# Performance work log

Measured on AMD Instinct MI355X. Metric: run time of the kernel, lower is better.

## Reference

```python
import jax, jax.numpy as jnp
import numpy as np

N, C, H, W, D = 2, 64, 256, 256, 2   # batch, dim, height, width, depth
NW, HEADS, TOPK, KVW = 8, 8, 4, 4    # n_win, num_heads, topk, kv_per_win


def _conv(x, w, b, pad, groups=1):
    # x: NCHW, w: OIHW
    y = jax.lax.conv_general_dilated(
        x, w, (1, 1), [(pad, pad), (pad, pad)],
        dimension_numbers=('NCHW', 'OIHW', 'NCHW'), feature_group_count=groups)
    return y if b is None else y + b[None, :, None, None]


def _ln(x, g, b):
    m = x.mean(-1, keepdims=True)
    v = ((x - m) ** 2).mean(-1, keepdims=True)
    return (x - m) * jax.lax.rsqrt(v + 1e-6) * g + b


def setup_inputs() -> dict:
    key = jax.random.key(0)
    ks = iter(jax.random.split(key, 32))
    def rn(shape, s=0.05):
        return jax.random.normal(next(ks), shape, jnp.float32) * s
    inp = {'x': jax.random.normal(next(ks), (N, C, H, W), jnp.float32)}
    inp.update(
        pos_w=rn((D, C, 1, 3, 3)), pos_b=jnp.zeros((D, C), jnp.float32),
        ln1_g=jnp.ones((D, C), jnp.float32), ln1_b=jnp.zeros((D, C), jnp.float32),
        qkv_w=rn((D, C, 3 * C)), qkv_b=jnp.zeros((D, 3 * C), jnp.float32),
        lepe_w=rn((D, C, 1, 5, 5)), lepe_b=jnp.zeros((D, C), jnp.float32),
        wo_w=rn((D, C, C)), wo_b=jnp.zeros((D, C), jnp.float32),
        ln2_g=jnp.ones((D, C), jnp.float32), ln2_b=jnp.zeros((D, C), jnp.float32),
        fc1_w=rn((D, C, 4 * C)), fc1_b=jnp.zeros((D, 4 * C), jnp.float32),
        pw_w=rn((D, 2 * C, 2 * C, 1, 1)),
        dw_w=rn((D, 2 * C, 1, 3, 3)), dw_b=jnp.zeros((D, 2 * C), jnp.float32),
        fc2_w=rn((D, 2 * C, C)), fc2_b=jnp.zeros((D, C), jnp.float32))
    return inp


def _attn(y, qkv_w, qkv_b, lepe_w, lepe_b, wo_w, wo_b):
    # Bi-level routing attention. y: NHWC
    n, h, w, c = y.shape
    hw, ww = h // NW, w // NW          # window size (32x32)
    p2 = NW * NW                        # number of windows (64)
    hd = c // HEADS
    scale = c ** -0.5                   # qk_dim ** -0.5
    qkv = y @ qkv_w + qkv_b             # (n,h,w,3c)
    q, kimg, vimg = jnp.split(qkv, 3, -1)

    def win(t):  # (n,h,w,c) -> (n,p2,hw,ww,c)
        return t.reshape(n, NW, hw, NW, ww, c).transpose(0, 1, 3, 2, 4, 5).reshape(n, p2, hw, ww, c)

    qw, kw, vw = win(q), win(kimg), win(vimg)
    # region-level routing: window-mean q/k, top-k windows per query window
    q_win = qw.mean((2, 3))
    k_win = kw.mean((2, 3))
    logits = jnp.einsum('npc,nqc->npq', q_win * scale, k_win)
    _, r_idx = jax.lax.top_k(logits, TOPK)           # (n,p2,topk) hard routing (mul_weight='none')
    # kv downsample: adaptive avg pool each 32x32 window to 4x4
    kv = jnp.concatenate([kw, vw], -1)               # (n,p2,hw,ww,2c)
    kvp = kv.reshape(n, p2, KVW, hw // KVW, KVW, ww // KVW, 2 * c).mean((3, 5))
    kvp = kvp.reshape(n, p2, KVW * KVW, 2 * c)       # (n,p2,16,2c)
    # gather top-k windows' kv tokens
    kv_sel = jax.vmap(lambda t, i: t[i])(kvp, r_idx)  # (n,p2,topk,16,2c)
    k_sel, v_sel = jnp.split(kv_sel, 2, -1)
    kt = TOPK * KVW * KVW                             # 64 kv tokens per window
    k_sel = k_sel.reshape(n, p2, kt, HEADS, hd)
    v_sel = v_sel.reshape(n, p2, kt, HEADS, hd)
    qp = qw.reshape(n, p2, hw * ww, HEADS, hd)
    att = jax.nn.softmax(jnp.einsum('npqhc,npkhc->nphqk', qp * scale, k_sel), -1)
    out = jnp.einsum('nphqk,npkhc->npqhc', att, v_sel).reshape(n, p2, hw, ww, c)
    out = out.reshape(n, NW, NW, hw, ww, c).transpose(0, 1, 3, 2, 4, 5).reshape(n, h, w, c)
    # LePE: depthwise 5x5 conv on v over the full image
    lepe = _conv(vimg.transpose(0, 3, 1, 2), lepe_w, lepe_b, 2, groups=c).transpose(0, 2, 3, 1)
    return (out + lepe) @ wo_w + wo_b


def _glu(y, fc1_w, fc1_b, pw_w, dw_w, dw_b, fc2_w, fc2_b):
    # BConvolutionalGLU. y: NHWC
    t = y @ fc1_w + fc1_b                 # (n,h,w,4c)
    xh, vh = jnp.split(t, 2, -1)          # each 2c
    xh = xh.transpose(0, 3, 1, 2)         # NCHW
    xh = _conv(xh, pw_w, None, 0)                           # BSConvU pointwise (no bias)
    xh = _conv(xh, dw_w, dw_b, 1, groups=dw_w.shape[0])     # BSConvU depthwise 3x3
    xh = jax.nn.gelu(xh, approximate=False) * vh.transpose(0, 3, 1, 2)
    return xh.transpose(0, 2, 3, 1) @ fc2_w + fc2_b


def reference(x, pos_w, pos_b, ln1_g, ln1_b, qkv_w, qkv_b, lepe_w, lepe_b,
              wo_w, wo_b, ln2_g, ln2_b, fc1_w, fc1_b, pw_w, dw_w, dw_b,
              fc2_w, fc2_b):
    for i in range(D):
        x = x + _conv(x, pos_w[i], pos_b[i], 1, groups=x.shape[1])
        y = x.transpose(0, 2, 3, 1)  # NHWC
        y = y + _attn(_ln(y, ln1_g[i], ln1_b[i]), qkv_w[i], qkv_b[i],
                      lepe_w[i], lepe_b[i], wo_w[i], wo_b[i])
        y = y + _glu(_ln(y, ln2_g[i], ln2_b[i]), fc1_w[i], fc1_b[i],
                     pw_w[i], dw_w[i], dw_b[i], fc2_w[i], fc2_b[i])
        x = y.transpose(0, 3, 1, 2)  # NCHW
    return x
```

## Files before the change

### kernel.cpp

```cpp
#include <hip/hip_runtime.h>
#include <hip/hip_bf16.h>

typedef __hip_bfloat16 bf16;
typedef __attribute__((ext_vector_type(8))) short short8v;
typedef __attribute__((ext_vector_type(4))) float f32x4;

static constexpr int Nn = 2, Hh = 256, Wd = 256;
static constexpr int Pp = Nn * Hh * Wd;

__device__ inline void sto(float* p, size_t i, float v) { p[i] = v; }
__device__ inline void sto(bf16* p, size_t i, float v) { p[i] = __float2bfloat16(v); }
__device__ inline void ld4(const float* p, float f[4]) {
  const float4 v = *(const float4*)p;
  f[0] = v.x; f[1] = v.y; f[2] = v.z; f[3] = v.w;
}
__device__ inline void ld4(const bf16* p, float f[4]) {
  uint2 u = *(const uint2*)p;
  f[0] = __uint_as_float(u.x << 16); f[1] = __uint_as_float(u.x & 0xffff0000u);
  f[2] = __uint_as_float(u.y << 16); f[3] = __uint_as_float(u.y & 0xffff0000u);
}
__device__ inline void st4(float* p, const float f[4]) {
  *(float4*)p = make_float4(f[0], f[1], f[2], f[3]);
}
__device__ inline void st4(bf16* p, const float f[4]) {
  union { bf16 h[4]; uint2 u; } x;
  x.h[0] = __float2bfloat16(f[0]); x.h[1] = __float2bfloat16(f[1]);
  x.h[2] = __float2bfloat16(f[2]); x.h[3] = __float2bfloat16(f[3]);
  *(uint2*)p = x.u;
}
__device__ inline uint2 pk4(float a, float b, float c, float d) {
  union { bf16 h[4]; uint2 u; } x;
  x.h[0] = __float2bfloat16(a); x.h[1] = __float2bfloat16(b);
  x.h[2] = __float2bfloat16(c); x.h[3] = __float2bfloat16(d);
  return x.u;
}

__global__ void __launch_bounds__(256) k_in_tr(const float* __restrict__ xin,
                                               float* __restrict__ X) {
  __shared__ float t[64][65];
  int blk = blockIdx.x;
  int wt = blk & 3, h = (blk >> 2) & 255, n = blk >> 10;
  int w0 = wt * 64;
  int tx = threadIdx.x & 63, ty = threadIdx.x >> 6;
  const float* src = xin + ((size_t)n * 64 * 256 + h) * 256 + w0;
#pragma unroll
  for (int cc = 0; cc < 16; cc++) {
    int c = cc * 4 + ty;
    t[c][tx] = src[(size_t)c * 65536 + tx];
  }
  __syncthreads();
  float* dst = X + (size_t)(n * 65536 + h * 256 + w0) * 64;
#pragma unroll
  for (int jj = 0; jj < 16; jj++) {
    int j = jj * 4 + ty;
    dst[(size_t)j * 64 + tx] = t[tx][j];
  }
}

__global__ void __launch_bounds__(256) k_out(const float* __restrict__ X,
                                             float* __restrict__ out) {
  __shared__ float t[64][65];
  int blk = blockIdx.x;
  int wt = blk & 3, h = (blk >> 2) & 255, n = blk >> 10;
  int w0 = wt * 64;
  int tx = threadIdx.x & 63, ty = threadIdx.x >> 6;
  const float* src = X + (size_t)(n * 65536 + h * 256 + w0) * 64;
#pragma unroll
  for (int jj = 0; jj < 16; jj++) {
    int j = jj * 4 + ty;
    t[tx][j] = src[(size_t)j * 64 + tx];
  }
  __syncthreads();
  float* dst = out + ((size_t)n * 64 * 256 + h) * 256 + w0;
#pragma unroll
  for (int cc = 0; cc < 16; cc++) {
    int c = cc * 4 + ty;
    dst[(size_t)c * 65536 + tx] = t[c][tx];
  }
}

__global__ void __launch_bounds__(256) k_pcln4(const float* __restrict__ X,
                                               float* __restrict__ A, float* __restrict__ T,
                                               bf16* __restrict__ Tb,
                                               const float* __restrict__ pw,
                                               const float* __restrict__ pb,
                                               const float* __restrict__ g,
                                               const float* __restrict__ b) {
  __shared__ float w9[9][68];
  __shared__ float bb[64];
  int tid = threadIdx.x;
  for (int j = tid; j < 576; j += 256) {
    int tap = j >> 6, c = j & 63;
    w9[tap][c] = pw[c * 9 + tap];
  }
  if (tid < 64) bb[tid] = pb[tid];
  __syncthreads();
  int gid = blockIdx.x * 256 + tid;
  int cg = gid & 15, pg = gid >> 4;
  int c0 = cg << 2;
  int w0 = (pg & 63) << 2, h = (pg >> 6) & 255, n = pg >> 14;
  int pbase = (n << 16) | (h << 8) | w0;
  float acc[4][4];
  {
    const float4 b4 = *(const float4*)&bb[c0];
#pragma unroll
    for (int px = 0; px < 4; px++) {
      acc[px][0] = b4.x; acc[px][1] = b4.y; acc[px][2] = b4.z; acc[px][3] = b4.w;
    }
  }
  float xc[4][4];
#pragma unroll
  for (int ky = 0; ky < 3; ky++) {
    int hh = h + ky - 1;
    if ((unsigned)hh >= 256u) continue;
    const float* xrow = X + (size_t)((n << 16) | (hh << 8)) * 64 + c0;
    float v[6][4];
#pragma unroll
    for (int dx = 0; dx < 6; dx++) {
      int ww = w0 + dx - 1;
      if ((unsigned)ww < 256u) ld4(xrow + (size_t)ww * 64, v[dx]);
      else { v[dx][0] = 0.f; v[dx][1] = 0.f; v[dx][2] = 0.f; v[dx][3] = 0.f; }
    }
    if (ky == 1) {
#pragma unroll
      for (int px = 0; px < 4; px++)
#pragma unroll
        for (int j = 0; j < 4; j++) xc[px][j] = v[px + 1][j];
    }
#pragma unroll
    for (int kx = 0; kx < 3; kx++) {
      const float4 wv = *(const float4*)&w9[ky * 3 + kx][c0];
#pragma unroll
      for (int px = 0; px < 4; px++) {
        acc[px][0] += wv.x * v[px + kx][0]; acc[px][1] += wv.y * v[px + kx][1];
        acc[px][2] += wv.z * v[px + kx][2]; acc[px][3] += wv.w * v[px + kx][3];
      }
    }
  }
  const float4 g4 = *(const float4*)&g[c0];
  const float4 b4 = *(const float4*)&b[c0];
#pragma unroll
  for (int px = 0; px < 4; px++) {
    float a[4];
#pragma unroll
    for (int j = 0; j < 4; j++) a[j] = xc[px][j] + acc[px][j];
    st4(A + (size_t)(pbase + px) * 64 + c0, a);
    float s = a[0] + a[1] + a[2] + a[3];
#pragma unroll
    for (int off = 8; off; off >>= 1) s += __shfl_xor(s, off);
    float mean = s * (1.f / 64.f);
    float d[4], q = 0.f;
#pragma unroll
    for (int j = 0; j < 4; j++) { d[j] = a[j] - mean; q += d[j] * d[j]; }
#pragma unroll
    for (int off = 8; off; off >>= 1) q += __shfl_xor(q, off);
    float inv = rsqrtf(q * (1.f / 64.f) + 1e-6f);
    float y[4] = {d[0] * inv * g4.x + b4.x, d[1] * inv * g4.y + b4.y,
                  d[2] * inv * g4.z + b4.z, d[3] * inv * g4.w + b4.w};
    st4(T + (size_t)(pbase + px) * 64 + c0, y);
    st4(Tb + (size_t)(pbase + px) * 64 + c0, y);
  }
}

__global__ void __launch_bounds__(256) k_lnb4(const float* __restrict__ In,
                                              bf16* __restrict__ Out,
                                              const float* __restrict__ g,
                                              const float* __restrict__ b) {
  int gid = blockIdx.x * 256 + threadIdx.x;
  int pix = gid >> 4, cq = (gid & 15) << 2;
  float a[4];
  ld4(In + (size_t)pix * 64 + cq, a);
  float s = a[0] + a[1] + a[2] + a[3];
#pragma unroll
  for (int off = 8; off; off >>= 1) s += __shfl_xor(s, off);
  float mean = s * (1.f / 64.f);
  float d[4], q = 0.f;
#pragma unroll
  for (int j = 0; j < 4; j++) { d[j] = a[j] - mean; q += d[j] * d[j]; }
#pragma unroll
  for (int off = 8; off; off >>= 1) q += __shfl_xor(q, off);
  float inv = rsqrtf(q * (1.f / 64.f) + 1e-6f);
  const float4 g4 = *(const float4*)&g[cq];
  const float4 b4 = *(const float4*)&b[cq];
  float y[4] = {d[0] * inv * g4.x + b4.x, d[1] * inv * g4.y + b4.y,
                d[2] * inv * g4.z + b4.z, d[3] * inv * g4.w + b4.w};
  st4(Out + (size_t)pix * 64 + cq, y);
}

__global__ void k_prep1(const float* __restrict__ qkvw, const float* __restrict__ qkvb,
                        const float* __restrict__ wow, const float* __restrict__ f2w,
                        bf16* __restrict__ WTq, bf16* __restrict__ WTo,
                        bf16* __restrict__ WT2, float* __restrict__ qbs) {
  int t = blockIdx.x * 256 + threadIdx.x;
  if (t < 8192) {
    int r = t >> 6, k = t & 63;
    int src = r < 64 ? r : r + 64;
    float v = qkvw[k * 192 + src];
    if (r < 64) v *= 0.125f;
    WTq[t] = __float2bfloat16(v);
  } else if (t < 12288) {
    int t2 = t - 8192;
    int r = t2 >> 6, k = t2 & 63;
    WTo[t2] = __float2bfloat16(wow[k * 64 + r]);
  } else if (t < 20480) {
    int t2 = t - 12288;
    int r = t2 >> 7, k = t2 & 127;
    WT2[t2] = __float2bfloat16(f2w[k * 64 + r]);
  }
  if (t < 64) qbs[t] = qkvb[t] * 0.125f;
}

__global__ void k_combine(const float* __restrict__ f1w, const float* __restrict__ f1b,
                          const float* __restrict__ pww, float* __restrict__ Wc,
                          float* __restrict__ bc) {
  int t = blockIdx.x * blockDim.x + threadIdx.x;
  if (t >= 8192) return;
  int o = t & 127, k = t >> 7;
  float acc = 0.f;
  for (int j = 0; j < 128; j++) acc += f1w[k * 256 + j] * pww[o * 128 + j];
  Wc[k * 128 + o] = acc;
  if (k == 0) {
    float b = 0.f;
    for (int j = 0; j < 128; j++) b += f1b[j] * pww[o * 128 + j];
    bc[o] = b;
  }
}

__global__ void k_prep2(const float* __restrict__ f1w, const float* __restrict__ Wc,
                        bf16* __restrict__ WTf1) {
  int t = blockIdx.x * 256 + threadIdx.x;
  if (t >= 16384) return;
  int r = t >> 6, k = t & 63;
  float v = r < 128 ? f1w[k * 256 + 128 + r] : Wc[k * 128 + (r - 128)];
  WTf1[t] = __float2bfloat16(v);
}

template <int K, int N1, int N2, typename TO1, typename TO2, bool RES>
__global__ void __launch_bounds__(256) k_mf(const bf16* __restrict__ In,
                                            const bf16* __restrict__ WT,
                                            const float* __restrict__ b1,
                                            const float* __restrict__ b2,
                                            const float* __restrict__ Res,
                                            TO1* __restrict__ O1, TO2* __restrict__ O2) {
  constexpr int NC = N1 + N2;
  constexpr int KS = K / 32;
  constexpr int NTW = NC / 64;
  constexpr int KB = K * 2;
  constexpr int CH = NC * K / 8;
  __shared__ char lw[NC * K * 2];
  int tid = threadIdx.x;
  for (int ch = tid; ch < CH; ch += 256) {
    int r = ch / (K / 8), cg = ch % (K / 8);
    int byte = (r * KB + cg * 16) ^ ((r & 7) << 4);
    *(uint4*)(lw + byte) = *(const uint4*)((const short*)WT + ch * 8);
  }
  __syncthreads();
  int wid = tid >> 6, lane = tid & 63;
  int lr = lane & 15, lg = lane >> 4;
  int mb = blockIdx.x * 128;
#pragma unroll 2
  for (int ms = 0; ms < 8; ms++) {
    int m0 = mb + ms * 16;
    short8v a[KS];
#pragma unroll
    for (int ks = 0; ks < KS; ks++)
      a[ks] = *(const short8v*)((const short*)In + (size_t)(m0 + lr) * K + ks * 32 + lg * 8);
#pragma unroll
    for (int t = 0; t < NTW; t++) {
      int nt = wid * NTW + t;
      int col = nt * 16 + lr;
      float bv = (N2 == 0 || col < N1) ? b1[col] : b2[col - N1];
      f32x4 acc = {bv, bv, bv, bv};
#pragma unroll
      for (int ks = 0; ks < KS; ks++) {
        int byte = (col * KB + ks * 64 + lg * 16) ^ ((col & 7) << 4);
        short8v bfrag = *(const short8v*)(lw + byte);
        acc = __builtin_amdgcn_mfma_f32_16x16x32_bf16(a[ks], bfrag, acc, 0, 0, 0);
      }
      int r0 = m0 + lg * 4;
#pragma unroll
      for (int j = 0; j < 4; j++) {
        float v = acc[j];
        size_t row = r0 + j;
        if (RES) v += Res[row * N1 + col];
        if (N2 == 0 || col < N1) sto(O1, row * N1 + col, v);
        else sto(O2, row * N2 + (col - N1), v);
      }
    }
  }
}

__global__ void k_pool8(const float* __restrict__ T, float* __restrict__ Y8) {
  int b = blockIdx.x;
  int c = threadIdx.x;
  int bx = b & 31, by = (b >> 5) & 31, n = b >> 10;
  float acc = 0.f;
  for (int r = 0; r < 8; r++)
    for (int s = 0; s < 8; s++) {
      int p = (n << 16) | ((by * 8 + r) << 8) | (bx * 8 + s);
      acc += T[(size_t)p * 64 + c];
    }
  Y8[(size_t)b * 64 + c] = acc * (1.f / 64.f);
}

__global__ void k_poolwin(const float* __restrict__ Y8, float* __restrict__ Ym) {
  int b = blockIdx.x;
  int c = threadIdx.x;
  int win = b & 63, n = b >> 6, wi = win >> 3, wj = win & 7;
  float acc = 0.f;
  for (int ti = 0; ti < 4; ti++)
    for (int tj = 0; tj < 4; tj++) {
      int y8 = (n * 32 + wi * 4 + ti) * 32 + wj * 4 + tj;
      acc += Y8[(size_t)y8 * 64 + c];
    }
  Ym[(size_t)b * 64 + c] = acc * (1.f / 16.f);
}

__global__ void k_qkwin(const float* __restrict__ Ym, const float* __restrict__ qw,
                        const float* __restrict__ qb, float* __restrict__ QW,
                        float* __restrict__ KW) {
  int t = blockIdx.x * blockDim.x + threadIdx.x;
  if (t >= 16384) return;
  int c = t & 63, row = (t >> 6) & 127, sel = t >> 13;
  const float* y = Ym + (size_t)row * 64;
  int col = sel * 64 + c;
  float acc = qb[col];
  for (int k = 0; k < 64; k++) acc += y[k] * qw[k * 192 + col];
  (sel ? KW : QW)[(size_t)row * 64 + c] = acc;
}

__global__ void k_kvp(const float* __restrict__ Y8, const float* __restrict__ qw,
                      const float* __restrict__ qb, float* __restrict__ KVP) {
  int t = blockIdx.x * blockDim.x + threadIdx.x;
  if (t >= 262144) return;
  int c2 = t & 127, tok = (t >> 7) & 15, win = (t >> 11) & 63, n = t >> 17;
  int wi = win >> 3, wj = win & 7, ti = tok >> 2, tj = tok & 3;
  int y8 = (n * 32 + wi * 4 + ti) * 32 + wj * 4 + tj;
  const float* y = Y8 + (size_t)y8 * 64;
  int col = 64 + c2;
  float acc = qb[col];
  for (int k = 0; k < 64; k++) acc += y[k] * qw[k * 192 + col];
  KVP[t] = acc;
}

__global__ void __launch_bounds__(64) k_route(const float* __restrict__ QW,
                                              const float* __restrict__ KW,
                                              int* __restrict__ RIDX) {
  __shared__ float kk[64][65];
  __shared__ float qq[64];
  int b = blockIdx.x;
  int lane = threadIdx.x;
  int n = b >> 6;
  qq[lane] = QW[(size_t)b * 64 + lane];
  for (int r = 0; r < 64; r++) kk[r][lane] = KW[(size_t)(n * 64 + r) * 64 + lane];
  __syncthreads();
  float t = 0.f;
  for (int c = 0; c < 64; c++) t += qq[c] * kk[lane][c];
  t *= 0.125f;
  int o0 = 0, o1 = 0, o2 = 0, o3 = 0;
#pragma unroll
  for (int j = 0; j < 4; j++) {
    float v = t; int idx = lane;
#pragma unroll
    for (int off = 32; off; off >>= 1) {
      float ov = __shfl_xor(v, off);
      int oi = __shfl_xor(idx, off);
      if (ov > v || (ov == v && oi < idx)) { v = ov; idx = oi; }
    }
    if (j == 0) o0 = idx; else if (j == 1) o1 = idx;
    else if (j == 2) o2 = idx; else o3 = idx;
    if (lane == idx) t = -1e30f;
  }
  if (lane == 0) {
    int* o = RIDX + (size_t)b * 4;
    o[0] = o0; o[1] = o1; o[2] = o2; o[3] = o3;
  }
}

__global__ void __launch_bounds__(256) k_attn_mf(const bf16* __restrict__ Qb,
                                                 const float* __restrict__ KVP,
                                                 const int* __restrict__ RIDX,
                                                 bf16* __restrict__ Sbf) {
  __shared__ bf16 ks[64][72];
  __shared__ bf16 vt[64][72];
  __shared__ bf16 pa[4][16][72];
  __shared__ float ldn[4][16];
  __shared__ int idx[4];
  int blk = blockIdx.x;
  int part = blk & 3, bw = blk >> 2;
  int n = bw >> 6, win = bw & 63;
  int tid = threadIdx.x;
  if (tid < 4) idx[tid] = RIDX[bw * 4 + tid];
  __syncthreads();
  {
    int tok = tid & 63;
    const float* src = KVP + ((size_t)(n * 64 + idx[tok >> 4]) * 16 + (tok & 15)) * 128;
    for (int cq = tid >> 6; cq < 16; cq += 4) {
      int c0 = cq * 4;
      const float4 k4 = *(const float4*)&src[c0];
      *(uint2*)&ks[tok][c0] = pk4(k4.x, k4.y, k4.z, k4.w);
      const float4 v4 = *(const float4*)&src[64 + c0];
      vt[c0 + 0][tok] = __float2bfloat16(v4.x);
      vt[c0 + 1][tok] = __float2bfloat16(v4.y);
      vt[c0 + 2][tok] = __float2bfloat16(v4.z);
      vt[c0 + 3][tok] = __float2bfloat16(v4.w);
    }
  }
  __syncthreads();
  int w = tid >> 6, lane = tid & 63;
  int lr = lane & 15, lg = lane >> 4;
  int wi = win >> 3, wj = win & 7;
  for (int it = 0; it < 4; it++) {
    int qbase = part * 256 + w * 64 + it * 16;
    int q_b = qbase + lr;
    int pix_b = (n << 16) | ((wi * 32 + (q_b >> 5)) << 8) | (wj * 32 + (q_b & 31));
    short8v qf0 = *(const short8v*)((const short*)Qb + (size_t)pix_b * 64 + lg * 8);
    short8v qf1 = *(const short8v*)((const short*)Qb + (size_t)pix_b * 64 + 32 + lg * 8);
    f32x4 p[4] = {{0,0,0,0},{0,0,0,0},{0,0,0,0},{0,0,0,0}};
#pragma unroll
    for (int mt = 0; mt < 4; mt++) {
      short8v a0 = *(const short8v*)&ks[mt * 16 + lr][lg * 8];
      p[mt] = __builtin_amdgcn_mfma_f32_16x16x32_bf16(a0, qf0, p[mt], 0, 0, 0);
    }
#pragma unroll
    for (int mt = 0; mt < 4; mt++) {
      short8v a1 = *(const short8v*)&ks[mt * 16 + lr][32 + lg * 8];
      p[mt] = __builtin_amdgcn_mfma_f32_16x16x32_bf16(a1, qf1, p[mt], 0, 0, 0);
    }
    float mx = -1e30f;
#pragma unroll
    for (int mt = 0; mt < 4; mt++)
#pragma unroll
      for (int j = 0; j < 4; j++) mx = fmaxf(mx, p[mt][j]);
    mx = fmaxf(mx, __shfl_xor(mx, 16));
    mx = fmaxf(mx, __shfl_xor(mx, 32));
    float e[4][4];
    float sum = 0.f;
#pragma unroll
    for (int mt = 0; mt < 4; mt++)
#pragma unroll
      for (int j = 0; j < 4; j++) { e[mt][j] = __expf(p[mt][j] - mx); sum += e[mt][j]; }
    sum += __shfl_xor(sum, 16);
    sum += __shfl_xor(sum, 32);
    if (lg == 0) ldn[w][lr] = sum;
#pragma unroll
    for (int mt = 0; mt < 4; mt++)
      *(uint2*)&pa[w][lr][mt * 16 + lg * 4] = pk4(e[mt][0], e[mt][1], e[mt][2], e[mt][3]);
    short8v pf0 = *(const short8v*)&pa[w][lr][lg * 8];
    short8v pf1 = *(const short8v*)&pa[w][lr][32 + lg * 8];
    f32x4 o4[4] = {{0,0,0,0},{0,0,0,0},{0,0,0,0},{0,0,0,0}};
#pragma unroll
    for (int nt = 0; nt < 4; nt++) {
      short8v v0 = *(const short8v*)&vt[nt * 16 + lr][lg * 8];
      o4[nt] = __builtin_amdgcn_mfma_f32_16x16x32_bf16(pf0, v0, o4[nt], 0, 0, 0);
    }
#pragma unroll
    for (int nt = 0; nt < 4; nt++) {
      short8v v1 = *(const short8v*)&vt[nt * 16 + lr][32 + lg * 8];
      o4[nt] = __builtin_amdgcn_mfma_f32_16x16x32_bf16(pf1, v1, o4[nt], 0, 0, 0);
    }
    float linv[4];
#pragma unroll
    for (int j = 0; j < 4; j++) linv[j] = 1.f / ldn[w][lg * 4 + j];
#pragma unroll
    for (int j = 0; j < 4; j++) {
      int q_o = qbase + lg * 4 + j;
      size_t pix_o = (n << 16) | ((wi * 32 + (q_o >> 5)) << 8) | (wj * 32 + (q_o & 31));
      bf16* op = Sbf + pix_o * 64 + lr;
#pragma unroll
      for (int nt = 0; nt < 4; nt++) op[nt * 16] = __float2bfloat16(o4[nt][j] * linv[j]);
    }
  }
}

__global__ void __launch_bounds__(256) k_lepe4(const bf16* __restrict__ V,
                                               const bf16* __restrict__ Sbf,
                                               bf16* __restrict__ Sb,
                                               const float* __restrict__ wt,
                                               const float* __restrict__ bs) {
  __shared__ float w5[25][68];
  __shared__ float bb[64];
  int tid = threadIdx.x;
  for (int j = tid; j < 1600; j += 256) {
    int tap = j >> 6, c = j & 63;
    w5[tap][c] = wt[c * 25 + tap];
  }
  if (tid < 64) bb[tid] = bs[tid];
  __syncthreads();
  int gid = blockIdx.x * 256 + tid;
  int cg = gid & 15, pg = gid >> 4;
  int c0 = cg << 2;
  int w0 = (pg & 63) << 2, h = (pg >> 6) & 255, n = pg >> 14;
  int pbase = (n << 16) | (h << 8) | w0;
  float acc[4][4];
  {
    const float4 b4 = *(const float4*)&bb[c0];
#pragma unroll
    for (int px = 0; px < 4; px++) {
      acc[px][0] = b4.x; acc[px][1] = b4.y; acc[px][2] = b4.z; acc[px][3] = b4.w;
    }
  }
#pragma unroll
  for (int ky = 0; ky < 5; ky++) {
    int hh = h + ky - 2;
    if ((unsigned)hh >= 256u) continue;
    const bf16* vrow = V + (size_t)((n << 16) | (hh << 8)) * 64 + c0;
    float v[8][4];
#pragma unroll
    for (int dx = 0; dx < 8; dx++) {
      int ww = w0 + dx - 2;
      if ((unsigned)ww < 256u) ld4(vrow + (size_t)ww * 64, v[dx]);
      else { v[dx][0] = 0.f; v[dx][1] = 0.f; v[dx][2] = 0.f; v[dx][3] = 0.f; }
    }
#pragma unroll
    for (int kx = 0; kx < 5; kx++) {
      const float4 wv = *(const float4*)&w5[ky * 5 + kx][c0];
#pragma unroll
      for (int px = 0; px < 4; px++) {
        acc[px][0] += wv.x * v[px + kx][0]; acc[px][1] += wv.y * v[px + kx][1];
        acc[px][2] += wv.z * v[px + kx][2]; acc[px][3] += wv.w * v[px + kx][3];
      }
    }
  }
#pragma unroll
  for (int px = 0; px < 4; px++) {
    float s4[4];
    ld4(Sbf + (size_t)(pbase + px) * 64 + c0, s4);
    float o[4] = {s4[0] + acc[px][0], s4[1] + acc[px][1],
                  s4[2] + acc[px][2], s4[3] + acc[px][3]};
    st4(Sb + (size_t)(pbase + px) * 64 + c0, o);
  }
}

__global__ void __launch_bounds__(256) k_gludw4(const bf16* __restrict__ PWO,
                                                const bf16* __restrict__ VH,
                                                const float* __restrict__ wt,
                                                const float* __restrict__ bs,
                                                bf16* __restrict__ G) {
  __shared__ float wd[9][132];
  __shared__ float bb[128];
  int tid = threadIdx.x;
  for (int j = tid; j < 1152; j += 256) {
    int tap = j >> 7, c = j & 127;
    wd[tap][c] = wt[c * 9 + tap];
  }
  if (tid < 128) bb[tid] = bs[tid];
  __syncthreads();
  int gid = blockIdx.x * 256 + tid;
  int cg = gid & 31, pg = gid >> 5;
  int c0 = cg << 2;
  int w0 = (pg & 63) << 2, h = (pg >> 6) & 255, n = pg >> 14;
  int pbase = (n << 16) | (h << 8) | w0;
  float acc[4][4];
  {
    const float4 b4 = *(const float4*)&bb[c0];
#pragma unroll
    for (int px = 0; px < 4; px++) {
      acc[px][0] = b4.x; acc[px][1] = b4.y; acc[px][2] = b4.z; acc[px][3] = b4.w;
    }
  }
#pragma unroll
  for (int ky = 0; ky < 3; ky++) {
    int hh = h + ky - 1;
    if ((unsigned)hh >= 256u) continue;
    const bf16* prow = PWO + (size_t)((n << 16) | (hh << 8)) * 128 + c0;
    float v[6][4];
#pragma unroll
    for (int dx = 0; dx < 6; dx++) {
      int ww = w0 + dx - 1;
      if ((unsigned)ww < 256u) ld4(prow + (size_t)ww * 128, v[dx]);
      else { v[dx][0] = 0.f; v[dx][1] = 0.f; v[dx][2] = 0.f; v[dx][3] = 0.f; }
    }
#pragma unroll
    for (int kx = 0; kx < 3; kx++) {
      const float4 wv = *(const float4*)&wd[ky * 3 + kx][c0];
#pragma unroll
      for (int px = 0; px < 4; px++) {
        acc[px][0] += wv.x * v[px + kx][0]; acc[px][1] += wv.y * v[px + kx][1];
        acc[px][2] += wv.z * v[px + kx][2]; acc[px][3] += wv.w * v[px + kx][3];
      }
    }
  }
#pragma unroll
  for (int px = 0; px < 4; px++) {
    float vh[4];
    ld4(VH + (size_t)(pbase + px) * 128 + c0, vh);
    float o[4];
#pragma unroll
    for (int j = 0; j < 4; j++) {
      float x = acc[px][j];
      float ge = 0.5f * x * (1.f + erff(x * 0.70710678118f));
      o[j] = ge * vh[j];
    }
    st4(G + (size_t)(pbase + px) * 128 + c0, o);
  }
}

extern "C" void kernel_launch(void* const* d_in, const int* in_sizes, int n_in,
                              void* d_out, int out_size, void* d_ws, size_t ws_size,
                              hipStream_t stream) {
  (void)in_sizes; (void)n_in; (void)out_size; (void)ws_size;
  const float* xin = (const float*)d_in[0];
  auto Wp = [&](int i) { return (const float*)d_in[i]; };
  char* ws = (char*)d_ws;
  const size_t MB = 1u << 20;
  float* X  = (float*)(ws + 0 * MB);
  float* A  = (float*)(ws + 32 * MB);
  float* T  = (float*)(ws + 64 * MB);
  char*  R  = ws + 96 * MB;
  char*  sm = ws + 128 * MB;
  size_t off = 0;
  auto alloc = [&](size_t bytes) {
    void* p = sm + off;
    off += (bytes + 255) & ~(size_t)255;
    return p;
  };
  float* Y8   = (float*)alloc(2 * 32 * 32 * 64 * 4);
  float* Ym   = (float*)alloc(2 * 64 * 64 * 4);
  float* QW   = (float*)alloc(2 * 64 * 64 * 4);
  float* KW   = (float*)alloc(2 * 64 * 64 * 4);
  float* KVP  = (float*)alloc(2 * 64 * 16 * 128 * 4);
  int*  RIDX  = (int*)alloc(2 * 64 * 4 * 4);
  float* Wc   = (float*)alloc(64 * 128 * 4);
  float* bc   = (float*)alloc(128 * 4);
  bf16* WTq   = (bf16*)alloc(128 * 64 * 2);
  bf16* WTo   = (bf16*)alloc(64 * 64 * 2);
  bf16* WT2   = (bf16*)alloc(64 * 128 * 2);
  bf16* WTf1  = (bf16*)alloc(256 * 64 * 2);
  float* qbs  = (float*)alloc(64 * 4);
  bf16* Vb   = (bf16*)R;
  bf16* Qb   = (bf16*)X;
  bf16* Tb   = (bf16*)(ws + 112 * MB);
  bf16* Sbf  = (bf16*)T;
  bf16* Sb   = Tb;
  bf16* PWO  = (bf16*)R;
  bf16* VH   = (bf16*)T;
  bf16* A2b  = (bf16*)A;
  bf16* G    = (bf16*)(ws + 48 * MB);

  k_in_tr<<<dim3(2048), dim3(256), 0, stream>>>(xin, X);
  for (int i = 0; i < 2; i++) {
    const float *posw = Wp(1) + i * 64 * 9, *posb = Wp(2) + i * 64;
    const float *l1g = Wp(3) + i * 64, *l1b = Wp(4) + i * 64;
    const float *qkvw = Wp(5) + i * 64 * 192, *qkvb = Wp(6) + i * 192;
    const float *lpw = Wp(7) + i * 64 * 25, *lpb = Wp(8) + i * 64;
    const float *wow = Wp(9) + i * 64 * 64, *wob = Wp(10) + i * 64;
    const float *l2g = Wp(11) + i * 64, *l2b = Wp(12) + i * 64;
    const float *f1w = Wp(13) + i * 64 * 256, *f1b = Wp(14) + i * 256;
    const float *pww = Wp(15) + i * 128 * 128;
    const float *dww = Wp(16) + i * 128 * 9, *dwb = Wp(17) + i * 128;
    const float *f2w = Wp(18) + i * 128 * 64, *f2b = Wp(19) + i * 64;

    k_prep1<<<dim3(80), dim3(256), 0, stream>>>(qkvw, qkvb, wow, f2w, WTq, WTo, WT2, qbs);
    k_pcln4<<<dim3(2048), dim3(256), 0, stream>>>(X, A, T, Tb, posw, posb, l1g, l1b);
    k_mf<64, 64, 64, bf16, bf16, false><<<dim3(Pp / 128), dim3(256), 0, stream>>>(
        Tb, WTq, qbs, qkvb + 128, nullptr, Qb, Vb);
    k_pool8<<<dim3(2048), dim3(64), 0, stream>>>(T, Y8);
    k_poolwin<<<dim3(128), dim3(64), 0, stream>>>(Y8, Ym);
    k_qkwin<<<dim3(64), dim3(256), 0, stream>>>(Ym, qkvw, qkvb, QW, KW);
    k_kvp<<<dim3(1024), dim3(256), 0, stream>>>(Y8, qkvw, qkvb, KVP);
    k_route<<<dim3(128), dim3(64), 0, stream>>>(QW, KW, RIDX);
    k_attn_mf<<<dim3(512), dim3(256), 0, stream>>>(Qb, KVP, RIDX, Sbf);
    k_lepe4<<<dim3(2048), dim3(256), 0, stream>>>(Vb, Sbf, Sb, lpw, lpb);
    k_mf<64, 64, 0, float, float, true><<<dim3(Pp / 128), dim3(256), 0, stream>>>(
        Sb, WTo, wob, nullptr, A, X, nullptr);
    k_lnb4<<<dim3(Pp / 16), dim3(256), 0, stream>>>(X, A2b, l2g, l2b);
    k_combine<<<dim3(32), dim3(256), 0, stream>>>(f1w, f1b, pww, Wc, bc);
    k_prep2<<<dim3(64), dim3(256), 0, stream>>>(f1w, Wc, WTf1);
    k_mf<64, 128, 128, bf16, bf16, false><<<dim3(Pp / 128), dim3(256), 0, stream>>>(
        A2b, WTf1, f1b + 128, bc, nullptr, VH, PWO);
    k_gludw4<<<dim3(4096), dim3(256), 0, stream>>>(PWO, VH, dww, dwb, G);
    k_mf<128, 64, 0, float, float, true><<<dim3(Pp / 128), dim3(256), 0, stream>>>(
        G, WT2, f2b, nullptr, X, X, nullptr);
  }
  k_out<<<dim3(2048), dim3(256), 0, stream>>>(X, (float*)d_out);
}
```

Measured before the change: 476.8 us.

## Fuse output projection with LayerNorm2, merge weight prep and window pooling kernels

Adds a kernel that runs the Wo projection plus residual and then applies LayerNorm2 in-block from shared memory, writing the bf16 LN output directly. This removes the separate LN pass that re-read X from global memory. All per-layer weight preparation (including the fused fc1/pointwise combine) now runs in a single kernel, and window pooling is merged into the q/k window projection, cutting several launches and the intermediate buffers. Workspace aliasing is reshuffled to fit the new buffers. The fused kernel adds two block barriers per 16-row step, which may cost some throughput in the projection.

```diff
diff --git a/kernel.cpp b/kernel.cpp
--- a/kernel.cpp
+++ b/kernel.cpp
@@ -162,35 +162,13 @@
   }
 }
 
-__global__ void __launch_bounds__(256) k_lnb4(const float* __restrict__ In,
-                                              bf16* __restrict__ Out,
-                                              const float* __restrict__ g,
-                                              const float* __restrict__ b) {
-  int gid = blockIdx.x * 256 + threadIdx.x;
-  int pix = gid >> 4, cq = (gid & 15) << 2;
-  float a[4];
-  ld4(In + (size_t)pix * 64 + cq, a);
-  float s = a[0] + a[1] + a[2] + a[3];
-#pragma unroll
-  for (int off = 8; off; off >>= 1) s += __shfl_xor(s, off);
-  float mean = s * (1.f / 64.f);
-  float d[4], q = 0.f;
-#pragma unroll
-  for (int j = 0; j < 4; j++) { d[j] = a[j] - mean; q += d[j] * d[j]; }
-#pragma unroll
-  for (int off = 8; off; off >>= 1) q += __shfl_xor(q, off);
-  float inv = rsqrtf(q * (1.f / 64.f) + 1e-6f);
-  const float4 g4 = *(const float4*)&g[cq];
-  const float4 b4 = *(const float4*)&b[cq];
-  float y[4] = {d[0] * inv * g4.x + b4.x, d[1] * inv * g4.y + b4.y,
-                d[2] * inv * g4.z + b4.z, d[3] * inv * g4.w + b4.w};
-  st4(Out + (size_t)pix * 64 + cq, y);
-}
-
-__global__ void k_prep1(const float* __restrict__ qkvw, const float* __restrict__ qkvb,
-                        const float* __restrict__ wow, const float* __restrict__ f2w,
-                        bf16* __restrict__ WTq, bf16* __restrict__ WTo,
-                        bf16* __restrict__ WT2, float* __restrict__ qbs) {
+__global__ void k_prep(const float* __restrict__ qkvw, const float* __restrict__ qkvb,
+                       const float* __restrict__ wow, const float* __restrict__ f2w,
+                       const float* __restrict__ f1w, const float* __restrict__ f1b,
+                       const float* __restrict__ pww,
+                       bf16* __restrict__ WTq, bf16* __restrict__ WTo,
+                       bf16* __restrict__ WT2, bf16* __restrict__ WTf1,
+                       float* __restrict__ qbs, float* __restrict__ bc) {
   int t = blockIdx.x * 256 + threadIdx.x;
   if (t < 8192) {
     int r = t >> 6, k = t & 63;
@@ -206,33 +184,23 @@
     int t2 = t - 12288;
     int r = t2 >> 7, k = t2 & 127;
     WT2[t2] = __float2bfloat16(f2w[k * 64 + r]);
+  } else if (t < 28672) {
+    int t2 = t - 20480;
+    int r = t2 >> 6, k = t2 & 63;
+    WTf1[t2] = __float2bfloat16(f1w[k * 256 + 128 + r]);
+  } else if (t < 36864) {
+    int t2 = t - 28672;
+    int o = t2 & 127, k = t2 >> 7;
+    float acc = 0.f;
+    for (int j = 0; j < 128; j++) acc += f1w[k * 256 + j] * pww[o * 128 + j];
+    WTf1[(128 + o) * 64 + k] = __float2bfloat16(acc);
+  } else if (t < 36992) {
+    int o = t - 36864;
+    float bv = 0.f;
+    for (int j = 0; j < 128; j++) bv += f1b[j] * pww[o * 128 + j];
+    bc[o] = bv;
   }
   if (t < 64) qbs[t] = qkvb[t] * 0.125f;
-}
-
-__global__ void k_combine(const float* __restrict__ f1w, const float* __restrict__ f1b,
-                          const float* __restrict__ pww, float* __restrict__ Wc,
-                          float* __restrict__ bc) {
-  int t = blockIdx.x * blockDim.x + threadIdx.x;
-  if (t >= 8192) return;
-  int o = t & 127, k = t >> 7;
-  float acc = 0.f;
-  for (int j = 0; j < 128; j++) acc += f1w[k * 256 + j] * pww[o * 128 + j];
-  Wc[k * 128 + o] = acc;
-  if (k == 0) {
-    float b = 0.f;
-    for (int j = 0; j < 128; j++) b += f1b[j] * pww[o * 128 + j];
-    bc[o] = b;
-  }
-}
-
-__global__ void k_prep2(const float* __restrict__ f1w, const float* __restrict__ Wc,
-                        bf16* __restrict__ WTf1) {
-  int t = blockIdx.x * 256 + threadIdx.x;
-  if (t >= 16384) return;
-  int r = t >> 6, k = t & 63;
-  float v = r < 128 ? f1w[k * 256 + 128 + r] : Wc[k * 128 + (r - 128)];
-  WTf1[t] = __float2bfloat16(v);
 }
 
 template <int K, int N1, int N2, typename TO1, typename TO2, bool RES>
@@ -290,6 +258,70 @@
   }
 }
 
+__global__ void __launch_bounds__(256) k_mf_wo_ln(const bf16* __restrict__ In,
+                                                  const bf16* __restrict__ WT,
+                                                  const float* __restrict__ bias,
+                                                  const float* __restrict__ Res,
+                                                  float* __restrict__ Xo,
+                                                  bf16* __restrict__ A2b,
+                                                  const float* __restrict__ g,
+                                                  const float* __restrict__ b) {
+  __shared__ char lw[64 * 64 * 2];
+  __shared__ float xs[16][68];
+  int tid = threadIdx.x;
+  for (int ch = tid; ch < 512; ch += 256) {
+    int r = ch >> 3, cg = ch & 7;
+    int byte = (r * 128 + cg * 16) ^ ((r & 7) << 4);
+    *(uint4*)(lw + byte) = *(const uint4*)((const short*)WT + ch * 8);
+  }
+  __syncthreads();
+  int wid = tid >> 6, lane = tid & 63;
+  int lr = lane & 15, lg = lane >> 4;
+  int col = wid * 16 + lr;
+  int mb = blockIdx.x * 128;
+  int row2 = tid >> 4, cq = (tid & 15) << 2;
+  const float4 g4 = *(const float4*)&g[cq];
+  const float4 b4 = *(const float4*)&b[cq];
+  float bv = bias[col];
+  for (int ms = 0; ms < 8; ms++) {
+    int m0 = mb + ms * 16;
+    short8v a0 = *(const short8v*)((const short*)In + (size_t)(m0 + lr) * 64 + lg * 8);
+    short8v a1 = *(const short8v*)((const short*)In + (size_t)(m0 + lr) * 64 + 32 + lg * 8);
+    f32x4 acc = {bv, bv, bv, bv};
+    {
+      int byte = (col * 128 + lg * 16) ^ ((col & 7) << 4);
+      acc = __builtin_amdgcn_mfma_f32_16x16x32_bf16(a0, *(const short8v*)(lw + byte), acc, 0, 0, 0);
+      byte = (col * 128 + 64 + lg * 16) ^ ((col & 7) << 4);
+      acc = __builtin_amdgcn_mfma_f32_16x16x32_bf16(a1, *(const short8v*)(lw + byte), acc, 0, 0, 0);
+    }
+    int r0 = m0 + lg * 4;
+#pragma unroll
+    for (int j = 0; j < 4; j++) {
+      float v = acc[j] + Res[(size_t)(r0 + j) * 64 + col];
+      Xo[(size_t)(r0 + j) * 64 + col] = v;
+      xs[lg * 4 + j][col] = v;
+    }
+    __syncthreads();
+    {
+      float a4[4] = {xs[row2][cq], xs[row2][cq + 1], xs[row2][cq + 2], xs[row2][cq + 3]};
+      float s = a4[0] + a4[1] + a4[2] + a4[3];
+#pragma unroll
+      for (int off = 8; off; off >>= 1) s += __shfl_xor(s, off);
+      float mean = s * (1.f / 64.f);
+      float d[4], q = 0.f;
+#pragma unroll
+      for (int j = 0; j < 4; j++) { d[j] = a4[j] - mean; q += d[j] * d[j]; }
+#pragma unroll
+      for (int off = 8; off; off >>= 1) q += __shfl_xor(q, off);
+      float inv = rsqrtf(q * (1.f / 64.f) + 1e-6f);
+      float y[4] = {d[0] * inv * g4.x + b4.x, d[1] * inv * g4.y + b4.y,
+                    d[2] * inv * g4.z + b4.z, d[3] * inv * g4.w + b4.w};
+      st4(A2b + (size_t)(m0 + row2) * 64 + cq, y);
+    }
+    __syncthreads();
+  }
+}
+
 __global__ void k_pool8(const float* __restrict__ T, float* __restrict__ Y8) {
   int b = blockIdx.x;
   int c = threadIdx.x;
@@ -303,29 +335,35 @@
   Y8[(size_t)b * 64 + c] = acc * (1.f / 64.f);
 }
 
-__global__ void k_poolwin(const float* __restrict__ Y8, float* __restrict__ Ym) {
-  int b = blockIdx.x;
-  int c = threadIdx.x;
-  int win = b & 63, n = b >> 6, wi = win >> 3, wj = win & 7;
-  float acc = 0.f;
-  for (int ti = 0; ti < 4; ti++)
-    for (int tj = 0; tj < 4; tj++) {
-      int y8 = (n * 32 + wi * 4 + ti) * 32 + wj * 4 + tj;
-      acc += Y8[(size_t)y8 * 64 + c];
-    }
-  Ym[(size_t)b * 64 + c] = acc * (1.f / 16.f);
-}
-
-__global__ void k_qkwin(const float* __restrict__ Ym, const float* __restrict__ qw,
-                        const float* __restrict__ qb, float* __restrict__ QW,
-                        float* __restrict__ KW) {
-  int t = blockIdx.x * blockDim.x + threadIdx.x;
-  if (t >= 16384) return;
-  int c = t & 63, row = (t >> 6) & 127, sel = t >> 13;
-  const float* y = Ym + (size_t)row * 64;
-  int col = sel * 64 + c;
-  float acc = qb[col];
-  for (int k = 0; k < 64; k++) acc += y[k] * qw[k * 192 + col];
+__global__ void __launch_bounds__(256) k_qkwin2(const float* __restrict__ Y8,
+                                                const float* __restrict__ qw,
+                                                const float* __restrict__ qb,
+                                                float* __restrict__ QW,
+                                                float* __restrict__ KW) {
+  __shared__ float ym[4][68];
+  int blk = blockIdx.x;
+  int sel = blk >> 5;
+  int r0 = (blk & 31) * 4;
+  int tid = threadIdx.x;
+  {
+    int rl = tid >> 6, c = tid & 63;
+    int row = r0 + rl;
+    int n = row >> 6, win = row & 63;
+    int wi = win >> 3, wj = win & 7;
+    float acc = 0.f;
+    for (int ti = 0; ti < 4; ti++)
+      for (int tj = 0; tj < 4; tj++) {
+        int y8 = (n * 32 + wi * 4 + ti) * 32 + wj * 4 + tj;
+        acc += Y8[(size_t)y8 * 64 + c];
+      }
+    ym[rl][c] = acc * (1.f / 16.f);
+  }
+  __syncthreads();
+  int rl = tid >> 6, c = tid & 63;
+  int row = r0 + rl;
+  int colg = sel * 64 + c;
+  float acc = qb[colg];
+  for (int k = 0; k < 64; k++) acc += ym[rl][k] * qw[k * 192 + colg];
   (sel ? KW : QW)[(size_t)row * 64 + c] = acc;
 }
 
@@ -607,7 +645,6 @@
   float* X  = (float*)(ws + 0 * MB);
   float* A  = (float*)(ws + 32 * MB);
   float* T  = (float*)(ws + 64 * MB);
-  char*  R  = ws + 96 * MB;
   char*  sm = ws + 128 * MB;
   size_t off = 0;
   auto alloc = [&](size_t bytes) {
@@ -616,27 +653,25 @@
     return p;
   };
   float* Y8   = (float*)alloc(2 * 32 * 32 * 64 * 4);
-  float* Ym   = (float*)alloc(2 * 64 * 64 * 4);
   float* QW   = (float*)alloc(2 * 64 * 64 * 4);
   float* KW   = (float*)alloc(2 * 64 * 64 * 4);
   float* KVP  = (float*)alloc(2 * 64 * 16 * 128 * 4);
   int*  RIDX  = (int*)alloc(2 * 64 * 4 * 4);
-  float* Wc   = (float*)alloc(64 * 128 * 4);
   float* bc   = (float*)alloc(128 * 4);
   bf16* WTq   = (bf16*)alloc(128 * 64 * 2);
   bf16* WTo   = (bf16*)alloc(64 * 64 * 2);
   bf16* WT2   = (bf16*)alloc(64 * 128 * 2);
   bf16* WTf1  = (bf16*)alloc(256 * 64 * 2);
   float* qbs  = (float*)alloc(64 * 4);
-  bf16* Vb   = (bf16*)R;
   bf16* Qb   = (bf16*)X;
+  bf16* Vb   = (bf16*)(ws + 96 * MB);
   bf16* Tb   = (bf16*)(ws + 112 * MB);
   bf16* Sbf  = (bf16*)T;
   bf16* Sb   = Tb;
-  bf16* PWO  = (bf16*)R;
-  bf16* VH   = (bf16*)T;
-  bf16* A2b  = (bf16*)A;
-  bf16* G    = (bf16*)(ws + 48 * MB);
+  bf16* A2b  = (bf16*)(ws + 96 * MB);
+  bf16* VH   = (bf16*)A;
+  bf16* PWO  = (bf16*)T;
+  bf16* G    = (bf16*)(ws + 96 * MB);
 
   k_in_tr<<<dim3(2048), dim3(256), 0, stream>>>(xin, X);
   for (int i = 0; i < 2; i++) {
@@ -651,22 +686,19 @@
     const float *dww = Wp(16) + i * 128 * 9, *dwb = Wp(17) + i * 128;
     const float *f2w = Wp(18) + i * 128 * 64, *f2b = Wp(19) + i * 64;
 
-    k_prep1<<<dim3(80), dim3(256), 0, stream>>>(qkvw, qkvb, wow, f2w, WTq, WTo, WT2, qbs);
+    k_prep<<<dim3(145), dim3(256), 0, stream>>>(qkvw, qkvb, wow, f2w, f1w, f1b, pww,
+                                                WTq, WTo, WT2, WTf1, qbs, bc);
     k_pcln4<<<dim3(2048), dim3(256), 0, stream>>>(X, A, T, Tb, posw, posb, l1g, l1b);
     k_mf<64, 64, 64, bf16, bf16, false><<<dim3(Pp / 128), dim3(256), 0, stream>>>(
         Tb, WTq, qbs, qkvb + 128, nullptr, Qb, Vb);
     k_pool8<<<dim3(2048), dim3(64), 0, stream>>>(T, Y8);
-    k_poolwin<<<dim3(128), dim3(64), 0, stream>>>(Y8, Ym);
-    k_qkwin<<<dim3(64), dim3(256), 0, stream>>>(Ym, qkvw, qkvb, QW, KW);
+    k_qkwin2<<<dim3(64), dim3(256), 0, stream>>>(Y8, qkvw, qkvb, QW, KW);
     k_kvp<<<dim3(1024), dim3(256), 0, stream>>>(Y8, qkvw, qkvb, KVP);
     k_route<<<dim3(128), dim3(64), 0, stream>>>(QW, KW, RIDX);
     k_attn_mf<<<dim3(512), dim3(256), 0, stream>>>(Qb, KVP, RIDX, Sbf);
     k_lepe4<<<dim3(2048), dim3(256), 0, stream>>>(Vb, Sbf, Sb, lpw, lpb);
-    k_mf<64, 64, 0, float, float, true><<<dim3(Pp / 128), dim3(256), 0, stream>>>(
-        Sb, WTo, wob, nullptr, A, X, nullptr);
-    k_lnb4<<<dim3(Pp / 16), dim3(256), 0, stream>>>(X, A2b, l2g, l2b);
-    k_combine<<<dim3(32), dim3(256), 0, stream>>>(f1w, f1b, pww, Wc, bc);
-    k_prep2<<<dim3(64), dim3(256), 0, stream>>>(f1w, Wc, WTf1);
+    k_mf_wo_ln<<<dim3(Pp / 128), dim3(256), 0, stream>>>(
+        Sb, WTo, wob, A, X, A2b, l2g, l2b);
     k_mf<64, 128, 128, bf16, bf16, false><<<dim3(Pp / 128), dim3(256), 0, stream>>>(
         A2b, WTf1, f1b + 128, bc, nullptr, VH, PWO);
     k_gludw4<<<dim3(4096), dim3(256), 0, stream>>>(PWO, VH, dww, dwb, G);
```

Result: faster. 448.7 us (-5.9%).
